# Kernel optimization log

Hardware: AMD Instinct MI355X
Metric: run time of the kernel (lower is better)

The kernel has to match this reference:

```python
import jax, jax.numpy as jnp
import numpy as np

B, S, E, H, C = 64, 512, 768, 768, 9
Q_GCE = 0.7
TAU = 0.7
IGNORE = -100


def setup_inputs() -> dict:
    key = jax.random.key(0)
    k_h, k_w1, k_w2, k_lab, k_drop = jax.random.split(key, 5)
    hidden = jax.random.normal(k_h, (B, S, E), dtype=jnp.float32)
    W1 = jax.random.normal(k_w1, (E, H), dtype=jnp.float32) * (1.0 / np.sqrt(E))
    b1 = jnp.zeros((H,), dtype=jnp.float32)
    W2 = jax.random.normal(k_w2, (H, C), dtype=jnp.float32) * (1.0 / np.sqrt(H))
    b2 = jnp.zeros((C,), dtype=jnp.float32)
    labels = jax.random.randint(k_lab, (B, S), 0, C, dtype=jnp.int64 if jax.config.jax_enable_x64 else jnp.int32)
    drop = jax.random.uniform(k_drop, (B, S)) < 0.1
    labels = jnp.where(drop, IGNORE, labels)
    return {"hidden": hidden, "W1": W1, "b1": b1, "W2": W2, "b2": b2,
            "labels": labels, "epoch": 5}


def reference(hidden, W1, b1, W2, b2, labels, epoch):
    # head: Linear -> Tanh -> Linear (dropout is identity at eval)
    h = jnp.tanh(jnp.einsum('bse,eh->bsh', hidden, W1) + b1)
    logit = jnp.einsum('bsh,hc->bsc', h, W2) + b2
    probs = jax.nn.softmax(logit, axis=2)  # [B,S,C]

    mask = labels != IGNORE
    safe_labels = jnp.where(mask, labels, 0)
    # p_i = probs[i, labels[i]] gathered for every token
    p = jnp.take_along_axis(probs, safe_labels[..., None], axis=2)[..., 0]  # [B,S]
    # GCE weight: w=1 for epoch<=2, else 1 if p>tau else 0 (constant wrt grads)
    w = jnp.where(epoch <= 2, 1.0, jnp.where(p > TAU, 1.0, 0.0))
    w = jax.lax.stop_gradient(w) * mask.astype(probs.dtype)
    loss = jnp.sum(w * (1.0 - jnp.power(p, Q_GCE)) / Q_GCE)
    return probs, loss
```

## Files before the change

### kernel.cpp

```cpp
#include <hip/hip_runtime.h>
#include <hip/hip_bf16.h>
#include <stdint.h>

#define E_ 768
#define H_ 768
#define C_ 9
#define M_TOTAL 32768

typedef __attribute__((ext_vector_type(8))) __bf16 bf16x8;
typedef __attribute__((ext_vector_type(4))) float f32x4;
typedef __attribute__((ext_vector_type(4))) int i32x4;

static_assert(sizeof(bf16x8) == 16, "bf16x8 must be 16B");

__device__ __forceinline__ unsigned short f2bf(float f) {
    __hip_bfloat16 h = __float2bfloat16(f);
    return __builtin_bit_cast(unsigned short, h);
}

__global__ void prep_kernel(const float* __restrict__ W1, const float* __restrict__ W2,
                            unsigned short* __restrict__ W1f, unsigned short* __restrict__ W2f,
                            float* __restrict__ loss_out)
{
    int tid = blockIdx.x * 256 + threadIdx.x;
    if (tid < 48 * 24 * 512) {
        int j    = tid & 7;
        int lane = (tid >> 3) & 63;
        int cell = tid >> 9;
        int t     = cell % 24;
        int ntile = cell / 24;
        int n = ntile * 16 + (lane & 15);
        int k = t * 32 + (lane >> 4) * 8 + j;
        W1f[tid] = f2bf(W1[k * H_ + n]);
    }
    if (tid < 24 * 512) {
        int j    = tid & 7;
        int lane = (tid >> 3) & 63;
        int t    = tid >> 9;
        int cls  = lane & 15;
        int k = t * 32 + (lane >> 4) * 8 + j;
        W2f[tid] = (cls < C_) ? f2bf(W2[k * C_ + cls]) : (unsigned short)0;
    }
    if (tid == 0) *loss_out = 0.0f;
}

__launch_bounds__(512, 2)
__global__ void fused_head_kernel(const float* __restrict__ hidden,
                                  const unsigned short* __restrict__ W1f,
                                  const float* __restrict__ b1,
                                  const unsigned short* __restrict__ W2f,
                                  const float* __restrict__ b2,
                                  const int* __restrict__ labels,
                                  const int* __restrict__ epoch_p,
                                  float* __restrict__ probs,
                                  float* __restrict__ loss)
{
    __shared__ unsigned short Ash[4 * 24 * 64 * 8];
    __shared__ unsigned short Hsh[8 * 4 * 64 * 8];

    const int tid  = threadIdx.x;
    const int w    = tid >> 6;
    const int lane = tid & 63;
    const int tok0 = blockIdx.x * 64;
    const int c16  = lane & 15;
    const int q    = lane >> 4;

#pragma unroll
    for (int i = 0; i < 12; ++i) {
        int cid  = i * 512 + tid;
        int cl   = cid & 63;
        int cell = cid >> 6;
        int t  = cell % 24;
        int mt = cell / 24;
        int row = tok0 + mt * 16 + (cl & 15);
        int k   = t * 32 + (cl >> 4) * 8;
        const float4* gp = (const float4*)(hidden + (size_t)row * E_ + k);
        float4 v0 = gp[0];
        float4 v1 = gp[1];
        union { unsigned short u[8]; i32x4 v; } pk;
        pk.u[0] = f2bf(v0.x); pk.u[1] = f2bf(v0.y);
        pk.u[2] = f2bf(v0.z); pk.u[3] = f2bf(v0.w);
        pk.u[4] = f2bf(v1.x); pk.u[5] = f2bf(v1.y);
        pk.u[6] = f2bf(v1.z); pk.u[7] = f2bf(v1.w);
        *(i32x4*)(&Ash[cid * 8]) = pk.v;
    }
    __syncthreads();

    const f32x4 zero4 = {0.0f, 0.0f, 0.0f, 0.0f};
    f32x4 logit = zero4;

    for (int c = 0; c < 3; ++c) {
        f32x4 acc[4][2];
#pragma unroll
        for (int mt = 0; mt < 4; ++mt)
#pragma unroll
            for (int nt = 0; nt < 2; ++nt)
                acc[mt][nt] = zero4;

        const unsigned short* bbase[2];
#pragma unroll
        for (int nt = 0; nt < 2; ++nt) {
            int ntile = c * 16 + w * 2 + nt;
            bbase[nt] = W1f + ((size_t)ntile * 24 * 64 + lane) * 8;
        }

#pragma unroll 8
        for (int t = 0; t < 24; ++t) {
            bf16x8 bfr[2], af[4];
#pragma unroll
            for (int nt = 0; nt < 2; ++nt)
                bfr[nt] = __builtin_bit_cast(bf16x8, *(const i32x4*)(bbase[nt] + t * 512));
#pragma unroll
            for (int mt = 0; mt < 4; ++mt)
                af[mt] = __builtin_bit_cast(bf16x8, *(const i32x4*)(&Ash[((mt * 24 + t) * 64 + lane) * 8]));
#pragma unroll
            for (int mt = 0; mt < 4; ++mt)
#pragma unroll
                for (int nt = 0; nt < 2; ++nt)
                    acc[mt][nt] = __builtin_amdgcn_mfma_f32_16x16x32_bf16(af[mt], bfr[nt], acc[mt][nt], 0, 0, 0);
        }

#pragma unroll
        for (int nt = 0; nt < 2; ++nt) {
            int kloc = w * 32 + nt * 16 + c16;
            int colg = c * 256 + kloc;
            float b1v = b1[colg];
            int t2 = kloc >> 5;
            int q2 = (kloc >> 3) & 3;
            int j  = kloc & 7;
#pragma unroll
            for (int mt = 0; mt < 4; ++mt) {
#pragma unroll
                for (int r = 0; r < 4; ++r) {
                    float z = acc[mt][nt][r] + b1v;
                    float e = exp2f(z * 2.8853900817779268f);
                    float th = 1.0f - 2.0f * __builtin_amdgcn_rcpf(e + 1.0f);
                    int lanep = (q * 4 + r) + 16 * q2;
                    Hsh[((t2 * 4 + mt) * 64 + lanep) * 8 + j] = f2bf(th);
                }
            }
        }
        __syncthreads();

        if (w < 4) {
#pragma unroll
            for (int t2 = 0; t2 < 8; ++t2) {
                bf16x8 ha = __builtin_bit_cast(bf16x8, *(const i32x4*)(&Hsh[((t2 * 4 + w) * 64 + lane) * 8]));
                bf16x8 wb = __builtin_bit_cast(bf16x8, *(const i32x4*)(W2f + ((size_t)(c * 8 + t2) * 64 + lane) * 8));
                logit = __builtin_amdgcn_mfma_f32_16x16x32_bf16(ha, wb, logit, 0, 0, 0);
            }
        }
        __syncthreads();
    }

    if (w < 4) {
        const bool valid = (c16 < C_);
        const float b2v = valid ? b2[c16] : 0.0f;
        const int ep = epoch_p[0];
        float lsum = 0.0f;
#pragma unroll
        for (int r = 0; r < 4; ++r) {
            float l = valid ? (logit[r] + b2v) : -3.0e38f;
            float m = l;
#pragma unroll
            for (int d = 1; d < 16; d <<= 1)
                m = fmaxf(m, __shfl_xor(m, d, 64));
            float e = valid ? exp2f((l - m) * 1.44269504f) : 0.0f;
            float s = e;
#pragma unroll
            for (int d = 1; d < 16; d <<= 1)
                s += __shfl_xor(s, d, 64);
            float p = e / s;
            int row = tok0 + w * 16 + q * 4 + r;
            if (valid) probs[(size_t)row * C_ + c16] = p;
            int lab = labels[row];
            if (valid && lab == c16) {
                float wgt = (ep <= 2) ? 1.0f : ((p > 0.7f) ? 1.0f : 0.0f);
                if (wgt > 0.0f)
                    lsum += (1.0f - exp2f(0.7f * log2f(p))) * (1.0f / 0.7f);
            }
        }
#pragma unroll
        for (int d = 1; d < 64; d <<= 1)
            lsum += __shfl_xor(lsum, d, 64);
        if (lane == 0) atomicAdd(loss, lsum);
    }
}

extern "C" void kernel_launch(void* const* d_in, const int* in_sizes, int n_in,
                              void* d_out, int out_size, void* d_ws, size_t ws_size,
                              hipStream_t stream)
{
    const float* hidden = (const float*)d_in[0];
    const float* W1     = (const float*)d_in[1];
    const float* b1     = (const float*)d_in[2];
    const float* W2     = (const float*)d_in[3];
    const float* b2     = (const float*)d_in[4];
    const int*   labels = (const int*)d_in[5];
    const int*   epoch  = (const int*)d_in[6];

    float* probs = (float*)d_out;
    float* loss  = probs + (size_t)M_TOTAL * C_;

    unsigned short* W1f = (unsigned short*)d_ws;
    unsigned short* W2f = W1f + 48 * 24 * 512;

    prep_kernel<<<2304, 256, 0, stream>>>(W1, W2, W1f, W2f, loss);
    fused_head_kernel<<<512, 512, 0, stream>>>(hidden, W1f, b1, W2f, b2,
                                               labels, epoch, probs, loss);
}
```

Measured before the change: 232.7 us.

## Double-buffer hidden tiles in LDS and compute full hidden width per pass

Instead of staging the whole 64x768 bf16 activation tile in LDS up front, the kernel now streams it in 96-column slabs through a double buffer, prefetching the next slab from global memory while MFMAs run on the current one. Each wave now owns 6 N-tiles (96 columns) over the whole K loop in a single pass, rather than looping three times over 2 N-tiles each. The tanh and second GEMM stage then proceed in four chunks of 192 columns. LDS use drops sharply and launch bounds rise to 4 blocks per CU, aiming for better occupancy and overlap of load latency, at the cost of a 96-float accumulator per thread, which risks register pressure or spills.

```diff
diff --git a/kernel.cpp b/kernel.cpp
--- a/kernel.cpp
+++ b/kernel.cpp
@@ -44,7 +44,7 @@
     if (tid == 0) *loss_out = 0.0f;
 }
 
-__launch_bounds__(512, 2)
+__launch_bounds__(512, 4)
 __global__ void fused_head_kernel(const float* __restrict__ hidden,
                                   const unsigned short* __restrict__ W1f,
                                   const float* __restrict__ b1,
@@ -55,8 +55,8 @@
                                   float* __restrict__ probs,
                                   float* __restrict__ loss)
 {
-    __shared__ unsigned short Ash[4 * 24 * 64 * 8];
-    __shared__ unsigned short Hsh[8 * 4 * 64 * 8];
+    __shared__ unsigned short Ast[2][4 * 3 * 512];
+    __shared__ unsigned short Hsh[6 * 4 * 512];
 
     const int tid  = threadIdx.x;
     const int w    = tid >> 6;
@@ -65,88 +65,110 @@
     const int c16  = lane & 15;
     const int q    = lane >> 4;
 
-#pragma unroll
-    for (int i = 0; i < 12; ++i) {
-        int cid  = i * 512 + tid;
-        int cl   = cid & 63;
-        int cell = cid >> 6;
-        int t  = cell % 24;
-        int mt = cell / 24;
-        int row = tok0 + mt * 16 + (cl & 15);
-        int k   = t * 32 + (cl >> 4) * 8;
-        const float4* gp = (const float4*)(hidden + (size_t)row * E_ + k);
-        float4 v0 = gp[0];
-        float4 v1 = gp[1];
-        union { unsigned short u[8]; i32x4 v; } pk;
-        pk.u[0] = f2bf(v0.x); pk.u[1] = f2bf(v0.y);
-        pk.u[2] = f2bf(v0.z); pk.u[3] = f2bf(v0.w);
-        pk.u[4] = f2bf(v1.x); pk.u[5] = f2bf(v1.y);
-        pk.u[6] = f2bf(v1.z); pk.u[7] = f2bf(v1.w);
-        *(i32x4*)(&Ash[cid * 8]) = pk.v;
+    const float* gsrc[3];
+    int swaddr[3];
+    #pragma unroll
+    for (int it = 0; it < 3; ++it) {
+        int idx = it * 512 + tid;
+        int tk  = idx / 24;
+        int kq  = idx - tk * 24;
+        int kl  = kq * 4;
+        int mt = tk >> 4, tl = kl >> 5;
+        int ln = (tk & 15) + 16 * ((kl >> 3) & 3);
+        swaddr[it] = ((mt * 3 + tl) * 64 + ln) * 8 + (kl & 7);
+        gsrc[it] = hidden + (size_t)(tok0 + tk) * E_ + kl;
+    }
+
+    uint32_t boff[6];
+    #pragma unroll
+    for (int i = 0; i < 6; ++i)
+        boff[i] = (uint32_t)(((w * 6 + i) * 24) * 64 + lane) * 8;
+
+    {
+        float4 v[3];
+        #pragma unroll
+        for (int it = 0; it < 3; ++it) v[it] = *(const float4*)(gsrc[it]);
+        #pragma unroll
+        for (int it = 0; it < 3; ++it) {
+            ushort4 u = { f2bf(v[it].x), f2bf(v[it].y), f2bf(v[it].z), f2bf(v[it].w) };
+            *(ushort4*)(&Ast[0][swaddr[it]]) = u;
+        }
     }
     __syncthreads();
 
     const f32x4 zero4 = {0.0f, 0.0f, 0.0f, 0.0f};
+    f32x4 acc[4][6];
+    #pragma unroll
+    for (int mt = 0; mt < 4; ++mt)
+        #pragma unroll
+        for (int i = 0; i < 6; ++i) acc[mt][i] = zero4;
+
+    #pragma unroll
+    for (int s = 0; s < 8; ++s) {
+        float4 v[3];
+        if (s < 7) {
+            #pragma unroll
+            for (int it = 0; it < 3; ++it)
+                v[it] = *(const float4*)(gsrc[it] + (s + 1) * 96);
+        }
+        const unsigned short* Ab = Ast[s & 1];
+        #pragma unroll
+        for (int tl = 0; tl < 3; ++tl) {
+            const int t = s * 3 + tl;
+            bf16x8 af[4], bfr[6];
+            #pragma unroll
+            for (int i = 0; i < 6; ++i)
+                bfr[i] = __builtin_bit_cast(bf16x8, *(const i32x4*)(W1f + boff[i] + t * 512));
+            #pragma unroll
+            for (int mt = 0; mt < 4; ++mt)
+                af[mt] = __builtin_bit_cast(bf16x8, *(const i32x4*)(&Ab[((mt * 3 + tl) * 64 + lane) * 8]));
+            #pragma unroll
+            for (int mt = 0; mt < 4; ++mt)
+                #pragma unroll
+                for (int i = 0; i < 6; ++i)
+                    acc[mt][i] = __builtin_amdgcn_mfma_f32_16x16x32_bf16(af[mt], bfr[i], acc[mt][i], 0, 0, 0);
+        }
+        if (s < 7) {
+            unsigned short* An = Ast[(s + 1) & 1];
+            #pragma unroll
+            for (int it = 0; it < 3; ++it) {
+                ushort4 u = { f2bf(v[it].x), f2bf(v[it].y), f2bf(v[it].z), f2bf(v[it].w) };
+                *(ushort4*)(&An[swaddr[it]]) = u;
+            }
+        }
+        __syncthreads();
+    }
+
     f32x4 logit = zero4;
-
-    for (int c = 0; c < 3; ++c) {
-        f32x4 acc[4][2];
-#pragma unroll
-        for (int mt = 0; mt < 4; ++mt)
-#pragma unroll
-            for (int nt = 0; nt < 2; ++nt)
-                acc[mt][nt] = zero4;
-
-        const unsigned short* bbase[2];
-#pragma unroll
-        for (int nt = 0; nt < 2; ++nt) {
-            int ntile = c * 16 + w * 2 + nt;
-            bbase[nt] = W1f + ((size_t)ntile * 24 * 64 + lane) * 8;
-        }
-
-#pragma unroll 8
-        for (int t = 0; t < 24; ++t) {
-            bf16x8 bfr[2], af[4];
-#pragma unroll
-            for (int nt = 0; nt < 2; ++nt)
-                bfr[nt] = __builtin_bit_cast(bf16x8, *(const i32x4*)(bbase[nt] + t * 512));
-#pragma unroll
-            for (int mt = 0; mt < 4; ++mt)
-                af[mt] = __builtin_bit_cast(bf16x8, *(const i32x4*)(&Ash[((mt * 24 + t) * 64 + lane) * 8]));
-#pragma unroll
-            for (int mt = 0; mt < 4; ++mt)
-#pragma unroll
-                for (int nt = 0; nt < 2; ++nt)
-                    acc[mt][nt] = __builtin_amdgcn_mfma_f32_16x16x32_bf16(af[mt], bfr[nt], acc[mt][nt], 0, 0, 0);
-        }
-
-#pragma unroll
-        for (int nt = 0; nt < 2; ++nt) {
-            int kloc = w * 32 + nt * 16 + c16;
-            int colg = c * 256 + kloc;
-            float b1v = b1[colg];
-            int t2 = kloc >> 5;
-            int q2 = (kloc >> 3) & 3;
-            int j  = kloc & 7;
-#pragma unroll
-            for (int mt = 0; mt < 4; ++mt) {
-#pragma unroll
-                for (int r = 0; r < 4; ++r) {
-                    float z = acc[mt][nt][r] + b1v;
-                    float e = exp2f(z * 2.8853900817779268f);
-                    float th = 1.0f - 2.0f * __builtin_amdgcn_rcpf(e + 1.0f);
-                    int lanep = (q * 4 + r) + 16 * q2;
-                    Hsh[((t2 * 4 + mt) * 64 + lanep) * 8 + j] = f2bf(th);
+    const int myc = w >> 1;
+    for (int c = 0; c < 4; ++c) {
+        if (myc == c) {
+            #pragma unroll
+            for (int i = 0; i < 6; ++i) {
+                int kloc = (w & 1) * 96 + i * 16 + c16;
+                float b1v = b1[c * 192 + kloc];
+                int t2 = kloc >> 5;
+                int q2 = (kloc >> 3) & 3;
+                int j  = kloc & 7;
+                #pragma unroll
+                for (int mt = 0; mt < 4; ++mt) {
+                    #pragma unroll
+                    for (int r = 0; r < 4; ++r) {
+                        float z = acc[mt][i][r] + b1v;
+                        float e = exp2f(z * 2.8853900817779268f);
+                        float th = 1.0f - 2.0f * __builtin_amdgcn_rcpf(e + 1.0f);
+                        int lanep = (q * 4 + r) + 16 * q2;
+                        Hsh[((t2 * 4 + mt) * 64 + lanep) * 8 + j] = f2bf(th);
+                    }
                 }
             }
         }
         __syncthreads();
-
         if (w < 4) {
-#pragma unroll
-            for (int t2 = 0; t2 < 8; ++t2) {
+            #pragma unroll
+            for (int t2 = 0; t2 < 6; ++t2) {
                 bf16x8 ha = __builtin_bit_cast(bf16x8, *(const i32x4*)(&Hsh[((t2 * 4 + w) * 64 + lane) * 8]));
-                bf16x8 wb = __builtin_bit_cast(bf16x8, *(const i32x4*)(W2f + ((size_t)(c * 8 + t2) * 64 + lane) * 8));
+                bf16x8 wb = __builtin_bit_cast(bf16x8, *(const i32x4*)(W2f + ((size_t)(c * 6 + t2) * 64 + lane) * 8));
                 logit = __builtin_amdgcn_mfma_f32_16x16x32_bf16(ha, wb, logit, 0, 0, 0);
             }
         }
@@ -158,16 +180,16 @@
         const float b2v = valid ? b2[c16] : 0.0f;
         const int ep = epoch_p[0];
         float lsum = 0.0f;
-#pragma unroll
+        #pragma unroll
         for (int r = 0; r < 4; ++r) {
             float l = valid ? (logit[r] + b2v) : -3.0e38f;
             float m = l;
-#pragma unroll
+            #pragma unroll
             for (int d = 1; d < 16; d <<= 1)
                 m = fmaxf(m, __shfl_xor(m, d, 64));
             float e = valid ? exp2f((l - m) * 1.44269504f) : 0.0f;
             float s = e;
-#pragma unroll
+            #pragma unroll
             for (int d = 1; d < 16; d <<= 1)
                 s += __shfl_xor(s, d, 64);
             float p = e / s;
@@ -180,7 +202,7 @@
                     lsum += (1.0f - exp2f(0.7f * log2f(p))) * (1.0f / 0.7f);
             }
         }
-#pragma unroll
+        #pragma unroll
         for (int d = 1; d < 64; d <<= 1)
             lsum += __shfl_xor(lsum, d, 64);
         if (lane == 0) atomicAdd(loss, lsum);
```

Result: slower. 387.0 us (+66.3%).
